# Kernel tuning notes

Hardware: AMD Instinct MI355X
Metric: run time of the kernel (lower is better)

The kernel has to match this reference:

```python
import jax, jax.numpy as jnp
import numpy as np

HIDDEN = 256
INPUT = 128
B, T = 256, 512
W_SCALE = 1.0 / np.sqrt(HIDDEN)  # matches PyTorch U(-1/sqrt(H), 1/sqrt(H)) magnitude


def setup_inputs() -> dict:
    key = jax.random.key(0)
    ks = jax.random.split(key, 5)
    x = jax.random.normal(ks[0], (B, T, INPUT), dtype=jnp.float32)
    W_ih = jax.random.normal(ks[1], (3 * HIDDEN, INPUT), dtype=jnp.float32) * W_SCALE
    W_hh = jax.random.normal(ks[2], (3 * HIDDEN, HIDDEN), dtype=jnp.float32) * W_SCALE
    b_ih = jax.random.normal(ks[3], (3 * HIDDEN,), dtype=jnp.float32) * W_SCALE
    b_hh = jax.random.normal(ks[4], (3 * HIDDEN,), dtype=jnp.float32) * W_SCALE
    return {"x": x, "W_ih": W_ih, "W_hh": W_hh, "b_ih": b_ih, "b_hh": b_hh}


def reference(x, W_ih, W_hh, b_ih, b_hh):
    # PyTorch GRU, gate order (r, z, n):
    #   r = sigmoid(W_ir x + b_ir + W_hr h + b_hr)
    #   z = sigmoid(W_iz x + b_iz + W_hz h + b_hz)
    #   n = tanh(W_in x + b_in + r * (W_hn h + b_hn))
    #   h' = (1 - z) * n + z * h
    Bsz = x.shape[0]
    H = W_hh.shape[1]
    # Precompute all input-to-gate projections once (big GEMM outside the scan).
    xg = jnp.einsum('bti,gi->btg', x, W_ih) + b_ih  # [B, T, 3H]

    def step(h, xg_t):
        hg = h @ W_hh.T + b_hh                      # [B, 3H]
        xr, xz, xn = jnp.split(xg_t, 3, axis=-1)
        hr, hz, hn = jnp.split(hg, 3, axis=-1)
        r = jax.nn.sigmoid(xr + hr)
        z = jax.nn.sigmoid(xz + hz)
        n = jnp.tanh(xn + r * hn)
        h_new = (1.0 - z) * n + z * h
        return h_new, h_new

    h0 = jnp.zeros((Bsz, H), dtype=x.dtype)
    _, hs = jax.lax.scan(step, h0, jnp.swapaxes(xg, 0, 1))  # hs: [T, B, H]
    return jnp.swapaxes(hs, 0, 1)                           # [B, T, H]
```

## Files before the change

### kernel.cpp

```cpp
#include <hip/hip_runtime.h>
#include <cstdint>
#include <cstddef>

typedef unsigned short u16;

#define HH 256
#define IIN 128
#define TT 512
#define G3 768

typedef __attribute__((ext_vector_type(8))) short bf16x8;
typedef __attribute__((ext_vector_type(4))) float f32x4;
typedef __attribute__((ext_vector_type(4))) int   i32x4;

__device__ __forceinline__ u16 f2bf(float f) {
    union { float f; uint32_t i; } c; c.f = f;
    uint32_t r = c.i + 0x7fffu + ((c.i >> 16) & 1u);
    return (u16)(r >> 16);
}
__device__ __forceinline__ float bf2f(u16 s) {
    union { uint32_t i; float f; } u; u.i = ((uint32_t)s) << 16; return u.f;
}
__device__ __forceinline__ float frcp(float x) { return __builtin_amdgcn_rcpf(x); }
__device__ __forceinline__ float sigm(float x) {
    float e = __expf(-fabsf(x));
    float s = frcp(1.f + e);
    return x >= 0.f ? s : 1.f - s;
}
__device__ __forceinline__ float tanh_f(float x) {
    float e = __expf(-2.f * fabsf(x));
    float t = (1.f - e) * frcp(1.f + e);
    return x >= 0.f ? t : -t;
}

#define LDS_BARRIER() asm volatile("s_waitcnt lgkmcnt(0)\n\ts_barrier" ::: "memory")

__global__ __launch_bounds__(256, 1) void xg_gemm(
    const float* __restrict__ x, const float* __restrict__ W_ih,
    const float* __restrict__ b_ih, const float* __restrict__ b_hh,
    u16* __restrict__ xg, int t0, int lt)
{
    __shared__ u16 xA[128 * 136];
    __shared__ u16 wB[3][128 * 136];
    __shared__ float biasS[384];
    const int tid = threadIdx.x;
    const int TcM = (1 << lt) - 1;
    const int srow = tid >> 5, sc = (tid & 31) * 4;
    const int lane = tid & 63, wv = tid >> 6;
    const int quad = lane >> 4, colL = lane & 15;

    #pragma unroll
    for (int w3 = 0; w3 < 3; ++w3) {
        const int n0 = blockIdx.y * 384 + w3 * 128;
        #pragma unroll
        for (int it = 0; it < 16; ++it) {
            int r = srow + it * 8;
            float4 wv4 = *(const float4*)(W_ih + (size_t)(n0 + r) * IIN + sc);
            ushort4 ws4 = { f2bf(wv4.x), f2bf(wv4.y), f2bf(wv4.z), f2bf(wv4.w) };
            *(ushort4*)&wB[w3][r * 136 + sc] = ws4;
        }
    }
    for (int n = tid; n < 384; n += 256) {
        int g = blockIdx.y * 384 + n;
        float bv = b_ih[g];
        if (g < 512) bv += b_hh[g];
        biasS[n] = bv;
    }

    for (int xt = 0; xt < 8; ++xt) {
        const int m0 = blockIdx.x * 1024 + xt * 128;
        if (xt) __syncthreads();
        #pragma unroll
        for (int it = 0; it < 16; ++it) {
            int r = srow + it * 8;
            int row = m0 + r;
            int b = row >> lt;
            int t = t0 + (row & TcM);
            float4 xv = *(const float4*)(x + ((size_t)b * TT + t) * IIN + sc);
            ushort4 xs = { f2bf(xv.x), f2bf(xv.y), f2bf(xv.z), f2bf(xv.w) };
            *(ushort4*)&xA[r * 136 + sc] = xs;
        }
        __syncthreads();

        #pragma unroll
        for (int w3 = 0; w3 < 3; ++w3) {
            f32x4 C[2][8] = {};
            #pragma unroll
            for (int kt = 0; kt < 4; ++kt) {
                bf16x8 A[2];
                #pragma unroll
                for (int i = 0; i < 2; ++i)
                    A[i] = *(const bf16x8*)&xA[(wv * 32 + i * 16 + colL) * 136 + kt * 32 + quad * 8];
                #pragma unroll
                for (int nn = 0; nn < 8; ++nn) {
                    bf16x8 Bf = *(const bf16x8*)&wB[w3][(nn * 16 + colL) * 136 + kt * 32 + quad * 8];
                    C[0][nn] = __builtin_amdgcn_mfma_f32_16x16x32_bf16(A[0], Bf, C[0][nn], 0, 0, 0);
                    C[1][nn] = __builtin_amdgcn_mfma_f32_16x16x32_bf16(A[1], Bf, C[1][nn], 0, 0, 0);
                }
            }
            #pragma unroll
            for (int i = 0; i < 2; ++i)
                #pragma unroll
                for (int nn = 0; nn < 8; ++nn) {
                    int cl = w3 * 128 + nn * 16 + colL;
                    float bv = biasS[cl];
                    #pragma unroll
                    for (int r = 0; r < 4; ++r) {
                        int row = m0 + wv * 32 + i * 16 + quad * 4 + r;
                        xg[(size_t)row * G3 + blockIdx.y * 384 + cl] = f2bf(C[i][nn][r] + bv);
                    }
                }
        }
    }
}

#define GRU_STEP(TC_, HBR_, HBW_, HQR_, HQW_, PR_, PZ_, PN_) do {              \
    f32x4 Cn[2] = {};                                                          \
    i32x4 Cr[2] = {}, Cz[2] = {};                                              \
    _Pragma("unroll")                                                          \
    for (int kt = 0; kt < 4; ++kt) {                                           \
        i32x4 Aq = *(const i32x4*)((const char*)(HQR_) + kt * 64 + quad * 16); \
        Cr[0] = __builtin_amdgcn_mfma_i32_16x16x64_i8(Aq, Br[0][kt], Cr[0], 0, 0, 0); \
        Cr[1] = __builtin_amdgcn_mfma_i32_16x16x64_i8(Aq, Br[1][kt], Cr[1], 0, 0, 0); \
        Cz[0] = __builtin_amdgcn_mfma_i32_16x16x64_i8(Aq, Bz[0][kt], Cz[0], 0, 0, 0); \
        Cz[1] = __builtin_amdgcn_mfma_i32_16x16x64_i8(Aq, Bz[1][kt], Cz[1], 0, 0, 0); \
    }                                                                          \
    _Pragma("unroll")                                                          \
    for (int kt = 0; kt < 8; ++kt) {                                           \
        bf16x8 A = *(const bf16x8*)&HBR_[kt * 32 + quad * 8];                  \
        Cn[0] = __builtin_amdgcn_mfma_f32_16x16x32_bf16(A, Bn[0][kt], Cn[0], 0, 0, 0); \
        Cn[1] = __builtin_amdgcn_mfma_f32_16x16x32_bf16(A, Bn[1][kt], Cn[1], 0, 0, 0); \
    }                                                                          \
    float dr = (float)(i16 ? Cr[1][0] : Cr[0][0]) * scR;                       \
    float dz = (float)(i16 ? Cz[1][0] : Cz[0][0]) * scZ;                       \
    float dn = i16 ? Cn[1][0] : Cn[0][0];                                      \
    float xr = PR_, xz = PZ_, xn = PN_;                                        \
    int t2 = (TC_) + 2; if (t2 > Tc - 1) t2 = Tc - 1;                          \
    const u16* p2 = xgb + (size_t)t2 * G3;                                     \
    PR_ = bf2f(p2[j]); PZ_ = bf2f(p2[256 + j]); PN_ = bf2f(p2[512 + j]);       \
    float r = sigm(xr + dr);                                                   \
    float z = sigm(xz + dz);                                                   \
    float n = tanh_f(xn + r * (dn + bhn));                                     \
    hreg = n + z * (hreg - n);                                                 \
    float hc = fminf(fmaxf(hreg, -1.f), 1.f);       \
    int hq8 = (int)rintf(hc * 127.f);                                          \
    if (lane < 32) {                                                           \
        HBW_[j] = f2bf(hreg);                                                  \
        ((char*)(HQW_))[j] = (char)hq8;                                        \
        outb[(size_t)(t0 + (TC_)) * HH + j] = hreg;                            \
    }                                                                          \
    LDS_BARRIER();                                                             \
} while (0)

__global__ __launch_bounds__(512, 1) void gru_seq(
    const float* __restrict__ W_hh, const float* __restrict__ b_hh,
    const u16* __restrict__ xg, float* __restrict__ out,
    float* __restrict__ hstate, int t0, int Tc)
{
    __shared__ __align__(16) u16 hBuf[2][HH];
    __shared__ __align__(16) int hqBuf[2][HH / 4];

    const int tid = threadIdx.x;
    const int lane = tid & 63, wv = tid >> 6;
    const int quad = lane >> 4, colL = lane & 15;
    const int i16 = quad & 1;
    const int j = wv * 32 + (lane & 31);
    const int b = blockIdx.x;

    bf16x8 Bn[2][8];
    #pragma unroll
    for (int i = 0; i < 2; ++i) {
        const size_t rowb = (size_t)(512 + wv * 32 + i * 16 + colL) * HH;
        #pragma unroll
        for (int kt = 0; kt < 8; ++kt) {
            float4 lo = *(const float4*)(W_hh + rowb + kt * 32 + quad * 8);
            float4 hi = *(const float4*)(W_hh + rowb + kt * 32 + quad * 8 + 4);
            union { bf16x8 v; u16 s[8]; } u;
            u.s[0] = f2bf(lo.x); u.s[1] = f2bf(lo.y);
            u.s[2] = f2bf(lo.z); u.s[3] = f2bf(lo.w);
            u.s[4] = f2bf(hi.x); u.s[5] = f2bf(hi.y);
            u.s[6] = f2bf(hi.z); u.s[7] = f2bf(hi.w);
            Bn[i][kt] = u.v;
        }
    }

    i32x4 Br[2][4], Bz[2][4];
    float scR = 0.f, scZ = 0.f;
    #pragma unroll
    for (int g = 0; g < 2; ++g) {
        #pragma unroll
        for (int i = 0; i < 2; ++i) {
            const float* wr = W_hh + (size_t)(g * 256 + wv * 32 + i * 16 + colL) * HH;
            float m = 0.f;
            #pragma unroll
            for (int kt = 0; kt < 4; ++kt)
                #pragma unroll
                for (int u4 = 0; u4 < 4; ++u4) {
                    float4 v = *(const float4*)(wr + kt * 64 + quad * 16 + u4 * 4);
                    m = fmaxf(m, fmaxf(fmaxf(fabsf(v.x), fabsf(v.y)),
                                       fmaxf(fabsf(v.z), fabsf(v.w))));
                }
            m = fmaxf(m, __shfl_xor(m, 16));
            m = fmaxf(m, __shfl_xor(m, 32));
            float inv = m > 1e-30f ? 127.f / m : 0.f;
            float sc  = m * (1.f / 16129.f);
            #pragma unroll
            for (int kt = 0; kt < 4; ++kt) {
                int pk[4];
                #pragma unroll
                for (int u4 = 0; u4 < 4; ++u4) {
                    float4 v = *(const float4*)(wr + kt * 64 + quad * 16 + u4 * 4);
                    int q0 = (int)rintf(fminf(fmaxf(v.x * inv, -127.f), 127.f));
                    int q1 = (int)rintf(fminf(fmaxf(v.y * inv, -127.f), 127.f));
                    int q2 = (int)rintf(fminf(fmaxf(v.z * inv, -127.f), 127.f));
                    int q3 = (int)rintf(fminf(fmaxf(v.w * inv, -127.f), 127.f));
                    pk[u4] = (q0 & 255) | ((q1 & 255) << 8) | ((q2 & 255) << 16) | (q3 << 24);
                }
                i32x4 t = { pk[0], pk[1], pk[2], pk[3] };
                if (g == 0) Br[i][kt] = t; else Bz[i][kt] = t;
            }
            if (i == i16) { if (g == 0) scR = sc; else scZ = sc; }
        }
    }

    float hreg = (t0 == 0) ? 0.f : hstate[b * HH + j];
    if (lane < 32) {
        hBuf[0][j] = f2bf(hreg);
        float hc = fminf(fmaxf(hreg, -1.f), 1.f);
        ((char*)hqBuf[0])[j] = (char)(int)rintf(hc * 127.f);
    }
    const float bhn = b_hh[512 + j];
    const u16* xgb = xg + (size_t)b * Tc * G3;
    float* outb = out + (size_t)b * TT * HH;

    float pr0 = bf2f(xgb[j]),      pz0 = bf2f(xgb[256 + j]),      pn0 = bf2f(xgb[512 + j]);
    float pr1 = bf2f(xgb[G3 + j]), pz1 = bf2f(xgb[G3 + 256 + j]), pn1 = bf2f(xgb[G3 + 512 + j]);
    __syncthreads();

    for (int tc = 0; tc < Tc; tc += 2) {
        GRU_STEP(tc,     hBuf[0], hBuf[1], hqBuf[0], hqBuf[1], pr0, pz0, pn0);
        GRU_STEP(tc + 1, hBuf[1], hBuf[0], hqBuf[1], hqBuf[0], pr1, pz1, pn1);
    }

    if (t0 + Tc < TT && lane < 32)
        hstate[b * HH + j] = hreg;
}

extern "C" void kernel_launch(void* const* d_in, const int* in_sizes, int n_in,
                              void* d_out, int out_size, void* d_ws, size_t ws_size,
                              hipStream_t stream) {
    const float* x    = (const float*)d_in[0];
    const float* W_ih = (const float*)d_in[1];
    const float* W_hh = (const float*)d_in[2];
    const float* b_ih = (const float*)d_in[3];
    const float* b_hh = (const float*)d_in[4];
    float* out = (float*)d_out;

    float* hstate = (float*)d_ws;
    u16* xg = (u16*)((char*)d_ws + 262144);
    size_t avail = ws_size > 262144 ? ws_size - 262144 : 0;

    int Tc = TT, lt = 9;
    while (Tc > 4 && (size_t)256 * Tc * G3 * 2 > avail) { Tc >>= 1; --lt; }

    for (int t0 = 0; t0 < TT; t0 += Tc) {
        xg_gemm<<<dim3(Tc / 4, 2), 256, 0, stream>>>(
            x, W_ih, b_ih, b_hh, xg, t0, lt);
        gru_seq<<<dim3(256), 512, 0, stream>>>(
            W_hh, b_hh, xg, out, hstate, t0, Tc);
    }
}
```

Before: 699.0 us.

## Load x fragments directly into registers in xg_gemm and double block size

The input-projection GEMM now has each wave load its A fragments straight from global memory into registers, converting them to bf16 in place. This removes the shared-memory staging of x and the per-tile barriers. The block grows from 256 to 512 threads, so eight waves cover 256 rows per pass over four passes. The cost is global reads in a per-lane gather pattern and higher register pressure. The recurrent kernel, which likely dominates runtime, is unchanged.

```diff
diff --git a/kernel.cpp b/kernel.cpp
--- a/kernel.cpp
+++ b/kernel.cpp
@@ -35,69 +35,74 @@
 
 #define LDS_BARRIER() asm volatile("s_waitcnt lgkmcnt(0)\n\ts_barrier" ::: "memory")
 
-__global__ __launch_bounds__(256, 1) void xg_gemm(
+__global__ __launch_bounds__(512, 1) void xg_gemm(
     const float* __restrict__ x, const float* __restrict__ W_ih,
     const float* __restrict__ b_ih, const float* __restrict__ b_hh,
     u16* __restrict__ xg, int t0, int lt)
 {
-    __shared__ u16 xA[128 * 136];
     __shared__ u16 wB[3][128 * 136];
     __shared__ float biasS[384];
     const int tid = threadIdx.x;
     const int TcM = (1 << lt) - 1;
-    const int srow = tid >> 5, sc = (tid & 31) * 4;
     const int lane = tid & 63, wv = tid >> 6;
     const int quad = lane >> 4, colL = lane & 15;
+    const int srow = tid >> 5, sc = (tid & 31) * 4;
 
     #pragma unroll
     for (int w3 = 0; w3 < 3; ++w3) {
         const int n0 = blockIdx.y * 384 + w3 * 128;
         #pragma unroll
-        for (int it = 0; it < 16; ++it) {
-            int r = srow + it * 8;
+        for (int it = 0; it < 8; ++it) {
+            int r = srow + it * 16;
             float4 wv4 = *(const float4*)(W_ih + (size_t)(n0 + r) * IIN + sc);
             ushort4 ws4 = { f2bf(wv4.x), f2bf(wv4.y), f2bf(wv4.z), f2bf(wv4.w) };
             *(ushort4*)&wB[w3][r * 136 + sc] = ws4;
         }
     }
-    for (int n = tid; n < 384; n += 256) {
-        int g = blockIdx.y * 384 + n;
+    if (tid < 384) {
+        int g = blockIdx.y * 384 + tid;
         float bv = b_ih[g];
         if (g < 512) bv += b_hh[g];
-        biasS[n] = bv;
-    }
-
-    for (int xt = 0; xt < 8; ++xt) {
-        const int m0 = blockIdx.x * 1024 + xt * 128;
-        if (xt) __syncthreads();
-        #pragma unroll
-        for (int it = 0; it < 16; ++it) {
-            int r = srow + it * 8;
-            int row = m0 + r;
+        biasS[tid] = bv;
+    }
+    __syncthreads();
+
+    const int colbase = blockIdx.y * 384;
+
+    for (int p = 0; p < 4; ++p) {
+        const int mrow = blockIdx.x * 1024 + p * 256 + wv * 32;
+
+        bf16x8 A[2][4];
+        #pragma unroll
+        for (int i = 0; i < 2; ++i) {
+            int row = mrow + i * 16 + colL;
             int b = row >> lt;
             int t = t0 + (row & TcM);
-            float4 xv = *(const float4*)(x + ((size_t)b * TT + t) * IIN + sc);
-            ushort4 xs = { f2bf(xv.x), f2bf(xv.y), f2bf(xv.z), f2bf(xv.w) };
-            *(ushort4*)&xA[r * 136 + sc] = xs;
-        }
-        __syncthreads();
+            const float* xr = x + ((size_t)b * TT + t) * IIN;
+            #pragma unroll
+            for (int kt = 0; kt < 4; ++kt) {
+                float4 lo = *(const float4*)(xr + kt * 32 + quad * 8);
+                float4 hi = *(const float4*)(xr + kt * 32 + quad * 8 + 4);
+                union { bf16x8 v; u16 s[8]; } u;
+                u.s[0] = f2bf(lo.x); u.s[1] = f2bf(lo.y);
+                u.s[2] = f2bf(lo.z); u.s[3] = f2bf(lo.w);
+                u.s[4] = f2bf(hi.x); u.s[5] = f2bf(hi.y);
+                u.s[6] = f2bf(hi.z); u.s[7] = f2bf(hi.w);
+                A[i][kt] = u.v;
+            }
+        }
 
         #pragma unroll
         for (int w3 = 0; w3 < 3; ++w3) {
             f32x4 C[2][8] = {};
             #pragma unroll
-            for (int kt = 0; kt < 4; ++kt) {
-                bf16x8 A[2];
-                #pragma unroll
-                for (int i = 0; i < 2; ++i)
-                    A[i] = *(const bf16x8*)&xA[(wv * 32 + i * 16 + colL) * 136 + kt * 32 + quad * 8];
+            for (int kt = 0; kt < 4; ++kt)
                 #pragma unroll
                 for (int nn = 0; nn < 8; ++nn) {
                     bf16x8 Bf = *(const bf16x8*)&wB[w3][(nn * 16 + colL) * 136 + kt * 32 + quad * 8];
-                    C[0][nn] = __builtin_amdgcn_mfma_f32_16x16x32_bf16(A[0], Bf, C[0][nn], 0, 0, 0);
-                    C[1][nn] = __builtin_amdgcn_mfma_f32_16x16x32_bf16(A[1], Bf, C[1][nn], 0, 0, 0);
-                }
-            }
+                    C[0][nn] = __builtin_amdgcn_mfma_f32_16x16x32_bf16(A[0][kt], Bf, C[0][nn], 0, 0, 0);
+                    C[1][nn] = __builtin_amdgcn_mfma_f32_16x16x32_bf16(A[1][kt], Bf, C[1][nn], 0, 0, 0);
+                }
             #pragma unroll
             for (int i = 0; i < 2; ++i)
                 #pragma unroll
@@ -106,8 +111,8 @@
                     float bv = biasS[cl];
                     #pragma unroll
                     for (int r = 0; r < 4; ++r) {
-                        int row = m0 + wv * 32 + i * 16 + quad * 4 + r;
-                        xg[(size_t)row * G3 + blockIdx.y * 384 + cl] = f2bf(C[i][nn][r] + bv);
+                        int row = mrow + i * 16 + quad * 4 + r;
+                        xg[(size_t)row * G3 + colbase + cl] = f2bf(C[i][nn][r] + bv);
                     }
                 }
         }
@@ -264,7 +269,7 @@
     while (Tc > 4 && (size_t)256 * Tc * G3 * 2 > avail) { Tc >>= 1; --lt; }
 
     for (int t0 = 0; t0 < TT; t0 += Tc) {
-        xg_gemm<<<dim3(Tc / 4, 2), 256, 0, stream>>>(
+        xg_gemm<<<dim3(Tc / 4, 2), 512, 0, stream>>>(
             x, W_ih, b_ih, b_hh, xg, t0, lt);
         gru_seq<<<dim3(256), 512, 0, stream>>>(
             W_hh, b_hh, xg, out, hstate, t0, Tc);
```

Result: slower. 713.1 us (+2.0%).
